# Kernel optimization log

Measured on AMD Instinct MI355X. Metric: run time of the kernel, lower is better.

## Reference

```python
import jax, jax.numpy as jnp
import numpy as np

N_NODES = 100000


def setup_inputs() -> dict:
    key = jax.random.key(0)
    k1, k2, k3 = jax.random.split(key, 3)
    x = jax.random.normal(k1, (N_NODES, 64), dtype=jnp.float32)
    edge_index = jax.random.randint(k2, (2, 1250000), 0, N_NODES, dtype=jnp.int64)
    W = jax.random.normal(k3, (128, 64), dtype=jnp.float32) * (1.0 / np.sqrt(128.0))
    b = jnp.zeros((64,), dtype=jnp.float32)
    return {"x": x, "edge_index": edge_index, "W": W, "b": b}


def reference(x, edge_index, W, b):
    n = x.shape[0]
    row, col = edge_index[0], edge_index[1]
    # scatter-add neighbor features onto destination nodes
    neigh = jax.ops.segment_sum(x[row], col, num_segments=n)          # [n, d]
    count = jax.ops.segment_sum(jnp.ones_like(col, dtype=x.dtype), col, num_segments=n)
    count = jnp.where(count == 0, jnp.asarray(1.0, x.dtype), count)   # avoid div-by-zero
    neigh = neigh / count[:, None]                                    # mean aggregation
    x_aggr = jnp.concatenate([x, neigh], axis=-1)                     # [n, 2d]
    out = x_aggr @ W + b                                              # [n, out_dim]
    return jax.nn.relu(out)  # dropout=0.0 (eval) -> identity
```

## Files before the change

### kernel.cpp

```cpp
#include <hip/hip_runtime.h>

#define D 64
#define NPB 64
#define THREADS 512
#define CAP 64

__device__ __forceinline__ unsigned short f2bf(float f) {
  unsigned u = __float_as_uint(f);
  return (unsigned short)((u + 0x7FFFu + ((u >> 16) & 1u)) >> 16);
}
__device__ __forceinline__ float bf2f(unsigned short h) {
  return __uint_as_float(((unsigned)h) << 16);
}

__global__ __launch_bounds__(256) void cvt_kernel(
    const float* __restrict__ x, ushort* __restrict__ xh, int total4) {
  int t = blockIdx.x * blockDim.x + threadIdx.x;
  if (t >= total4) return;
  float4 v = ((const float4*)x)[t];
  ushort4 h;
  h.x = f2bf(v.x); h.y = f2bf(v.y); h.z = f2bf(v.z); h.w = f2bf(v.w);
  ((ushort4*)xh)[t] = h;
}

__global__ __launch_bounds__(256) void fill_xcd_kernel(
    const int* __restrict__ ei, int* __restrict__ cnt,
    int* __restrict__ bucket, int e, int qpc) {
  const int myx = blockIdx.x & 7;
  const int chunk = blockIdx.x >> 3;
  const int quads = e >> 2;
  const int4* row4 = (const int4*)ei;
  const int4* col4 = (const int4*)(ei + e);
  int qend = chunk * qpc + qpc;
  if (qend > quads) qend = quads;
  for (int q = chunk * qpc + threadIdx.x; q < qend; q += 256) {
    int4 r = row4[q];
    int4 c = col4[q];
    if (((c.x >> 11) & 7) == myx) {
      int p = atomicAdd(&cnt[c.x], 1);
      if (p < CAP) bucket[(size_t)c.x * CAP + p] = r.x;
    }
    if (((c.y >> 11) & 7) == myx) {
      int p = atomicAdd(&cnt[c.y], 1);
      if (p < CAP) bucket[(size_t)c.y * CAP + p] = r.y;
    }
    if (((c.z >> 11) & 7) == myx) {
      int p = atomicAdd(&cnt[c.z], 1);
      if (p < CAP) bucket[(size_t)c.z * CAP + p] = r.z;
    }
    if (((c.w >> 11) & 7) == myx) {
      int p = atomicAdd(&cnt[c.w], 1);
      if (p < CAP) bucket[(size_t)c.w * CAP + p] = r.w;
    }
  }
}

__global__ __launch_bounds__(THREADS, 8) void fused_bf_kernel(
    const float* __restrict__ x, const ushort* __restrict__ xh,
    const int* __restrict__ cnt, const float* __restrict__ W,
    const float* __restrict__ b, float* __restrict__ out, int n) {
  __shared__ __align__(16) float xs[NPB * 128];

  const int lane = threadIdx.x & 63;
  const int wid  = threadIdx.x >> 6;
  const int base = blockIdx.x * NPB;
  const int* bucket = (const int*)out;

  for (int m = 0; m < 8; ++m) {
    int nl = wid * 8 + m;
    int node = base + nl;
    if (node < n) {
      int dg = cnt[node];
      int dc = dg < CAP ? dg : CAP;
      int bk = bucket[(size_t)node * CAP + lane];
      float xown = x[(size_t)node * D + lane];
      float s0 = 0.f, s1 = 0.f, s2 = 0.f, s3 = 0.f;
      float s4 = 0.f, s5 = 0.f, s6 = 0.f, s7 = 0.f;
      int p = 0;
      for (; p + 8 <= dc; p += 8) {
        int a0 = __shfl(bk, p),     a1 = __shfl(bk, p + 1);
        int a2 = __shfl(bk, p + 2), a3 = __shfl(bk, p + 3);
        int a4 = __shfl(bk, p + 4), a5 = __shfl(bk, p + 5);
        int a6 = __shfl(bk, p + 6), a7 = __shfl(bk, p + 7);
        ushort h0 = xh[(size_t)a0 * D + lane];
        ushort h1 = xh[(size_t)a1 * D + lane];
        ushort h2 = xh[(size_t)a2 * D + lane];
        ushort h3 = xh[(size_t)a3 * D + lane];
        ushort h4 = xh[(size_t)a4 * D + lane];
        ushort h5 = xh[(size_t)a5 * D + lane];
        ushort h6 = xh[(size_t)a6 * D + lane];
        ushort h7 = xh[(size_t)a7 * D + lane];
        s0 += bf2f(h0); s1 += bf2f(h1); s2 += bf2f(h2); s3 += bf2f(h3);
        s4 += bf2f(h4); s5 += bf2f(h5); s6 += bf2f(h6); s7 += bf2f(h7);
      }
      for (; p + 4 <= dc; p += 4) {
        int a0 = __shfl(bk, p),     a1 = __shfl(bk, p + 1);
        int a2 = __shfl(bk, p + 2), a3 = __shfl(bk, p + 3);
        ushort h0 = xh[(size_t)a0 * D + lane];
        ushort h1 = xh[(size_t)a1 * D + lane];
        ushort h2 = xh[(size_t)a2 * D + lane];
        ushort h3 = xh[(size_t)a3 * D + lane];
        s0 += bf2f(h0); s1 += bf2f(h1); s2 += bf2f(h2); s3 += bf2f(h3);
      }
      for (; p < dc; ++p)
        s0 += bf2f(xh[(size_t)__shfl(bk, p) * D + lane]);
      float sum = ((s0 + s1) + (s2 + s3)) + ((s4 + s5) + (s6 + s7));
      float inv = (dg > 0) ? (1.0f / (float)dg) : 0.0f;
      xs[nl * 128 + lane]      = xown;
      xs[nl * 128 + 64 + lane] = sum * inv;
    } else {
      xs[nl * 128 + lane]      = 0.0f;
      xs[nl * 128 + 64 + lane] = 0.0f;
    }
  }
  __syncthreads();

  const int col = lane;
  float bias = b[col];
  float acc[8];
#pragma unroll
  for (int m = 0; m < 8; ++m) acc[m] = bias;

  for (int k = 0; k < 128; k += 4) {
    float w0 = W[(k + 0) * 64 + col];
    float w1 = W[(k + 1) * 64 + col];
    float w2 = W[(k + 2) * 64 + col];
    float w3 = W[(k + 3) * 64 + col];
#pragma unroll
    for (int m = 0; m < 8; ++m) {
      int nl = wid + m * 8;
      float4 xv = *(const float4*)&xs[nl * 128 + k];
      acc[m] = fmaf(xv.x, w0, acc[m]);
      acc[m] = fmaf(xv.y, w1, acc[m]);
      acc[m] = fmaf(xv.z, w2, acc[m]);
      acc[m] = fmaf(xv.w, w3, acc[m]);
    }
  }

#pragma unroll
  for (int m = 0; m < 8; ++m) {
    int node = base + wid + m * 8;
    if (node < n)
      out[(size_t)node * D + col] = fmaxf(acc[m], 0.0f);
  }
}

__global__ __launch_bounds__(256) void fill_cap_kernel(
    const int* __restrict__ ei, int* __restrict__ cnt,
    int* __restrict__ bucket, int e) {
  int t = blockIdx.x * blockDim.x + threadIdx.x;
  if (t * 4 >= e) return;
  int4 r4 = ((const int4*)ei)[t];
  int4 c4 = ((const int4*)(ei + e))[t];
  int p0 = atomicAdd(&cnt[c4.x], 1);
  int p1 = atomicAdd(&cnt[c4.y], 1);
  int p2 = atomicAdd(&cnt[c4.z], 1);
  int p3 = atomicAdd(&cnt[c4.w], 1);
  if (p0 < CAP) bucket[(size_t)c4.x * CAP + p0] = r4.x;
  if (p1 < CAP) bucket[(size_t)c4.y * CAP + p1] = r4.y;
  if (p2 < CAP) bucket[(size_t)c4.z * CAP + p2] = r4.z;
  if (p3 < CAP) bucket[(size_t)c4.w * CAP + p3] = r4.w;
}

__global__ __launch_bounds__(THREADS, 8) void fused_cap_kernel(
    const float* __restrict__ x, const int* __restrict__ cnt,
    const float* __restrict__ W, const float* __restrict__ b,
    float* __restrict__ out, int n) {
  __shared__ __align__(16) float xs[NPB * 128];
  const int lane = threadIdx.x & 63;
  const int wid  = threadIdx.x >> 6;
  const int base = blockIdx.x * NPB;
  const int* bucket = (const int*)out;

  for (int m = 0; m < 8; ++m) {
    int nl = wid * 8 + m;
    int node = base + nl;
    if (node < n) {
      int dg = cnt[node];
      int dc = dg < CAP ? dg : CAP;
      int bk = bucket[(size_t)node * CAP + lane];
      float xown = x[(size_t)node * D + lane];
      float s0 = 0.f, s1 = 0.f, s2 = 0.f, s3 = 0.f;
      float s4 = 0.f, s5 = 0.f, s6 = 0.f, s7 = 0.f;
      int p = 0;
      for (; p + 8 <= dc; p += 8) {
        int a0 = __shfl(bk, p),     a1 = __shfl(bk, p + 1);
        int a2 = __shfl(bk, p + 2), a3 = __shfl(bk, p + 3);
        int a4 = __shfl(bk, p + 4), a5 = __shfl(bk, p + 5);
        int a6 = __shfl(bk, p + 6), a7 = __shfl(bk, p + 7);
        s0 += x[(size_t)a0 * D + lane];
        s1 += x[(size_t)a1 * D + lane];
        s2 += x[(size_t)a2 * D + lane];
        s3 += x[(size_t)a3 * D + lane];
        s4 += x[(size_t)a4 * D + lane];
        s5 += x[(size_t)a5 * D + lane];
        s6 += x[(size_t)a6 * D + lane];
        s7 += x[(size_t)a7 * D + lane];
      }
      for (; p + 4 <= dc; p += 4) {
        int a0 = __shfl(bk, p),     a1 = __shfl(bk, p + 1);
        int a2 = __shfl(bk, p + 2), a3 = __shfl(bk, p + 3);
        s0 += x[(size_t)a0 * D + lane];
        s1 += x[(size_t)a1 * D + lane];
        s2 += x[(size_t)a2 * D + lane];
        s3 += x[(size_t)a3 * D + lane];
      }
      for (; p < dc; ++p)
        s0 += x[(size_t)__shfl(bk, p) * D + lane];
      float sum = ((s0 + s1) + (s2 + s3)) + ((s4 + s5) + (s6 + s7));
      float inv = (dg > 0) ? (1.0f / (float)dg) : 0.0f;
      xs[nl * 128 + lane]      = xown;
      xs[nl * 128 + 64 + lane] = sum * inv;
    } else {
      xs[nl * 128 + lane]      = 0.0f;
      xs[nl * 128 + 64 + lane] = 0.0f;
    }
  }
  __syncthreads();

  const int col = lane;
  float bias = b[col];
  float acc[8];
#pragma unroll
  for (int m = 0; m < 8; ++m) acc[m] = bias;
  for (int k = 0; k < 128; k += 4) {
    float w0 = W[(k + 0) * 64 + col];
    float w1 = W[(k + 1) * 64 + col];
    float w2 = W[(k + 2) * 64 + col];
    float w3 = W[(k + 3) * 64 + col];
#pragma unroll
    for (int m = 0; m < 8; ++m) {
      int nl = wid + m * 8;
      float4 xv = *(const float4*)&xs[nl * 128 + k];
      acc[m] = fmaf(xv.x, w0, acc[m]);
      acc[m] = fmaf(xv.y, w1, acc[m]);
      acc[m] = fmaf(xv.z, w2, acc[m]);
      acc[m] = fmaf(xv.w, w3, acc[m]);
    }
  }
#pragma unroll
  for (int m = 0; m < 8; ++m) {
    int node = base + wid + m * 8;
    if (node < n)
      out[(size_t)node * D + col] = fmaxf(acc[m], 0.0f);
  }
}

extern "C" void kernel_launch(void* const* d_in, const int* in_sizes, int n_in,
                              void* d_out, int out_size, void* d_ws, size_t ws_size,
                              hipStream_t stream) {
  const float* x = (const float*)d_in[0];
  const int* ei = (const int*)d_in[1];
  const float* W = (const float*)d_in[2];
  const float* b = (const float*)d_in[3];
  float* out = (float*)d_out;

  int n = in_sizes[0] / D;
  int e = in_sizes[1] / 2;
  int nblocks = (n + NPB - 1) / NPB;

  size_t xh_bytes = (size_t)n * D * sizeof(ushort);
  size_t need = xh_bytes + (size_t)n * sizeof(int) + 256;

  if (ws_size >= need && (e & 3) == 0 && n <= (1 << 17)) {
    ushort* xh = (ushort*)d_ws;
    int* cnt = (int*)((char*)d_ws + ((xh_bytes + 255) & ~(size_t)255));

    int total4 = n * D / 4;
    cvt_kernel<<<(total4 + 255) / 256, 256, 0, stream>>>(x, xh, total4);

    hipMemsetAsync(cnt, 0, (size_t)n * sizeof(int), stream);

    int quads = e >> 2;
    int qpc = (quads + 255) / 256;
    fill_xcd_kernel<<<256 * 8, 256, 0, stream>>>(ei, cnt, (int*)d_out, e, qpc);

    fused_bf_kernel<<<nblocks, THREADS, 0, stream>>>(x, xh, cnt, W, b, out, n);
  } else {
    int* cnt = (int*)d_ws;
    hipMemsetAsync(cnt, 0, (size_t)n * sizeof(int), stream);
    int quads = e / 4;
    fill_cap_kernel<<<(quads + 255) / 256, 256, 0, stream>>>(ei, cnt, (int*)d_out, e);
    fused_cap_kernel<<<nblocks, THREADS, 0, stream>>>(x, cnt, W, b, out, n);
  }
}
```

Measured before the change: 210.1 us.

## Merge prep stages into cooperative kernel and gather two bf16 features per lane

Replaces the separate bf16 conversion kernel, count memset and bucket-fill kernel with one cooperative prep kernel that zeroes counts and converts x, then does a grid-wide sync before filling buckets. This removes two launches and a memset. The gather loop now has each half-wavefront load a 32-bit pair of bf16 values for a different neighbor, so each wave covers two neighbors per load and halves the load instruction count, then combines the halves with a cross-lane xor shuffle. The fallback path drops its 8-way unroll. Risks include the cost of the grid sync, a smaller grid now handling the bucket fill, and per-call occupancy and attribute queries on the host.

```diff
diff --git a/kernel.cpp b/kernel.cpp
--- a/kernel.cpp
+++ b/kernel.cpp
@@ -1,4 +1,7 @@
 #include <hip/hip_runtime.h>
+#include <hip/hip_cooperative_groups.h>
+
+namespace cg = cooperative_groups;
 
 #define D 64
 #define NPB 64
@@ -9,23 +12,25 @@
   unsigned u = __float_as_uint(f);
   return (unsigned short)((u + 0x7FFFu + ((u >> 16) & 1u)) >> 16);
 }
-__device__ __forceinline__ float bf2f(unsigned short h) {
-  return __uint_as_float(((unsigned)h) << 16);
-}
-
-__global__ __launch_bounds__(256) void cvt_kernel(
-    const float* __restrict__ x, ushort* __restrict__ xh, int total4) {
-  int t = blockIdx.x * blockDim.x + threadIdx.x;
-  if (t >= total4) return;
-  float4 v = ((const float4*)x)[t];
-  ushort4 h;
-  h.x = f2bf(v.x); h.y = f2bf(v.y); h.z = f2bf(v.z); h.w = f2bf(v.w);
-  ((ushort4*)xh)[t] = h;
-}
-
-__global__ __launch_bounds__(256) void fill_xcd_kernel(
-    const int* __restrict__ ei, int* __restrict__ cnt,
-    int* __restrict__ bucket, int e, int qpc) {
+
+__global__ __launch_bounds__(256) void prep_kernel(
+    const float* __restrict__ x, const int* __restrict__ ei,
+    ushort* __restrict__ xh, int* __restrict__ cnt,
+    int* __restrict__ bucket, int n, int e, int qpc) {
+  cg::grid_group grid = cg::this_grid();
+  const int tid = blockIdx.x * 256 + threadIdx.x;
+  const int nth = gridDim.x * 256;
+
+  for (int i = tid; i < n; i += nth) cnt[i] = 0;
+  const int total4 = n * D / 4;
+  for (int i = tid; i < total4; i += nth) {
+    float4 v = ((const float4*)x)[i];
+    ushort4 h;
+    h.x = f2bf(v.x); h.y = f2bf(v.y); h.z = f2bf(v.z); h.w = f2bf(v.w);
+    ((ushort4*)xh)[i] = h;
+  }
+  grid.sync();
+
   const int myx = blockIdx.x & 7;
   const int chunk = blockIdx.x >> 3;
   const int quads = e >> 2;
@@ -55,7 +60,7 @@
   }
 }
 
-__global__ __launch_bounds__(THREADS, 8) void fused_bf_kernel(
+__global__ __launch_bounds__(THREADS, 8) void fused2_kernel(
     const float* __restrict__ x, const ushort* __restrict__ xh,
     const int* __restrict__ cnt, const float* __restrict__ W,
     const float* __restrict__ b, float* __restrict__ out, int n) {
@@ -64,7 +69,10 @@
   const int lane = threadIdx.x & 63;
   const int wid  = threadIdx.x >> 6;
   const int base = blockIdx.x * NPB;
+  const int half = lane >> 5;
+  const int fl   = lane & 31;
   const int* bucket = (const int*)out;
+  const ushort* xp = xh + fl * 2;
 
   for (int m = 0; m < 8; ++m) {
     int nl = wid * 8 + m;
@@ -74,40 +82,49 @@
       int dc = dg < CAP ? dg : CAP;
       int bk = bucket[(size_t)node * CAP + lane];
       float xown = x[(size_t)node * D + lane];
-      float s0 = 0.f, s1 = 0.f, s2 = 0.f, s3 = 0.f;
-      float s4 = 0.f, s5 = 0.f, s6 = 0.f, s7 = 0.f;
+      float sl0 = 0.f, sl1 = 0.f, sl2 = 0.f, sl3 = 0.f;
+      float sh0 = 0.f, sh1 = 0.f, sh2 = 0.f, sh3 = 0.f;
       int p = 0;
       for (; p + 8 <= dc; p += 8) {
-        int a0 = __shfl(bk, p),     a1 = __shfl(bk, p + 1);
-        int a2 = __shfl(bk, p + 2), a3 = __shfl(bk, p + 3);
-        int a4 = __shfl(bk, p + 4), a5 = __shfl(bk, p + 5);
-        int a6 = __shfl(bk, p + 6), a7 = __shfl(bk, p + 7);
-        ushort h0 = xh[(size_t)a0 * D + lane];
-        ushort h1 = xh[(size_t)a1 * D + lane];
-        ushort h2 = xh[(size_t)a2 * D + lane];
-        ushort h3 = xh[(size_t)a3 * D + lane];
-        ushort h4 = xh[(size_t)a4 * D + lane];
-        ushort h5 = xh[(size_t)a5 * D + lane];
-        ushort h6 = xh[(size_t)a6 * D + lane];
-        ushort h7 = xh[(size_t)a7 * D + lane];
-        s0 += bf2f(h0); s1 += bf2f(h1); s2 += bf2f(h2); s3 += bf2f(h3);
-        s4 += bf2f(h4); s5 += bf2f(h5); s6 += bf2f(h6); s7 += bf2f(h7);
-      }
-      for (; p + 4 <= dc; p += 4) {
-        int a0 = __shfl(bk, p),     a1 = __shfl(bk, p + 1);
-        int a2 = __shfl(bk, p + 2), a3 = __shfl(bk, p + 3);
-        ushort h0 = xh[(size_t)a0 * D + lane];
-        ushort h1 = xh[(size_t)a1 * D + lane];
-        ushort h2 = xh[(size_t)a2 * D + lane];
-        ushort h3 = xh[(size_t)a3 * D + lane];
-        s0 += bf2f(h0); s1 += bf2f(h1); s2 += bf2f(h2); s3 += bf2f(h3);
-      }
-      for (; p < dc; ++p)
-        s0 += bf2f(xh[(size_t)__shfl(bk, p) * D + lane]);
-      float sum = ((s0 + s1) + (s2 + s3)) + ((s4 + s5) + (s6 + s7));
+        int a0 = __shfl(bk, p + 0 + half);
+        int a1 = __shfl(bk, p + 2 + half);
+        int a2 = __shfl(bk, p + 4 + half);
+        int a3 = __shfl(bk, p + 6 + half);
+        unsigned h0 = *(const unsigned*)(xp + (size_t)a0 * D);
+        unsigned h1 = *(const unsigned*)(xp + (size_t)a1 * D);
+        unsigned h2 = *(const unsigned*)(xp + (size_t)a2 * D);
+        unsigned h3 = *(const unsigned*)(xp + (size_t)a3 * D);
+        sl0 += __uint_as_float(h0 << 16);
+        sh0 += __uint_as_float(h0 & 0xffff0000u);
+        sl1 += __uint_as_float(h1 << 16);
+        sh1 += __uint_as_float(h1 & 0xffff0000u);
+        sl2 += __uint_as_float(h2 << 16);
+        sh2 += __uint_as_float(h2 & 0xffff0000u);
+        sl3 += __uint_as_float(h3 << 16);
+        sh3 += __uint_as_float(h3 & 0xffff0000u);
+      }
+      for (; p + 2 <= dc; p += 2) {
+        int a = __shfl(bk, p + half);
+        unsigned h = *(const unsigned*)(xp + (size_t)a * D);
+        sl0 += __uint_as_float(h << 16);
+        sh0 += __uint_as_float(h & 0xffff0000u);
+      }
+      if (p < dc) {
+        int a = __shfl(bk, p);
+        if (half == 0) {
+          unsigned h = *(const unsigned*)(xp + (size_t)a * D);
+          sl0 += __uint_as_float(h << 16);
+          sh0 += __uint_as_float(h & 0xffff0000u);
+        }
+      }
+      float sl = (sl0 + sl1) + (sl2 + sl3);
+      float sh = (sh0 + sh1) + (sh2 + sh3);
+      sl += __shfl_xor(sl, 32);
+      sh += __shfl_xor(sh, 32);
       float inv = (dg > 0) ? (1.0f / (float)dg) : 0.0f;
-      xs[nl * 128 + lane]      = xown;
-      xs[nl * 128 + 64 + lane] = sum * inv;
+      xs[nl * 128 + lane] = xown;
+      if (half == 0)
+        *(float2*)&xs[nl * 128 + 64 + fl * 2] = make_float2(sl * inv, sh * inv);
     } else {
       xs[nl * 128 + lane]      = 0.0f;
       xs[nl * 128 + 64 + lane] = 0.0f;
@@ -181,22 +198,7 @@
       int bk = bucket[(size_t)node * CAP + lane];
       float xown = x[(size_t)node * D + lane];
       float s0 = 0.f, s1 = 0.f, s2 = 0.f, s3 = 0.f;
-      float s4 = 0.f, s5 = 0.f, s6 = 0.f, s7 = 0.f;
       int p = 0;
-      for (; p + 8 <= dc; p += 8) {
-        int a0 = __shfl(bk, p),     a1 = __shfl(bk, p + 1);
-        int a2 = __shfl(bk, p + 2), a3 = __shfl(bk, p + 3);
-        int a4 = __shfl(bk, p + 4), a5 = __shfl(bk, p + 5);
-        int a6 = __shfl(bk, p + 6), a7 = __shfl(bk, p + 7);
-        s0 += x[(size_t)a0 * D + lane];
-        s1 += x[(size_t)a1 * D + lane];
-        s2 += x[(size_t)a2 * D + lane];
-        s3 += x[(size_t)a3 * D + lane];
-        s4 += x[(size_t)a4 * D + lane];
-        s5 += x[(size_t)a5 * D + lane];
-        s6 += x[(size_t)a6 * D + lane];
-        s7 += x[(size_t)a7 * D + lane];
-      }
       for (; p + 4 <= dc; p += 4) {
         int a0 = __shfl(bk, p),     a1 = __shfl(bk, p + 1);
         int a2 = __shfl(bk, p + 2), a3 = __shfl(bk, p + 3);
@@ -207,7 +209,7 @@
       }
       for (; p < dc; ++p)
         s0 += x[(size_t)__shfl(bk, p) * D + lane];
-      float sum = ((s0 + s1) + (s2 + s3)) + ((s4 + s5) + (s6 + s7));
+      float sum = (s0 + s1) + (s2 + s3);
       float inv = (dg > 0) ? (1.0f / (float)dg) : 0.0f;
       xs[nl * 128 + lane]      = xown;
       xs[nl * 128 + 64 + lane] = sum * inv;
@@ -266,16 +268,24 @@
     ushort* xh = (ushort*)d_ws;
     int* cnt = (int*)((char*)d_ws + ((xh_bytes + 255) & ~(size_t)255));
 
-    int total4 = n * D / 4;
-    cvt_kernel<<<(total4 + 255) / 256, 256, 0, stream>>>(x, xh, total4);
-
-    hipMemsetAsync(cnt, 0, (size_t)n * sizeof(int), stream);
+    int occ = 8, ncu = 256;
+    hipOccupancyMaxActiveBlocksPerMultiprocessor(&occ, prep_kernel, 256, 0);
+    hipDeviceGetAttribute(&ncu, hipDeviceAttributeMultiprocessorCount, 0);
+    long long cap = (long long)occ * ncu;
+    int grid = (int)(cap < 2048 ? cap : 2048);
+    grid &= ~7;
+    if (grid < 8) grid = 8;
 
     int quads = e >> 2;
-    int qpc = (quads + 255) / 256;
-    fill_xcd_kernel<<<256 * 8, 256, 0, stream>>>(ei, cnt, (int*)d_out, e, qpc);
-
-    fused_bf_kernel<<<nblocks, THREADS, 0, stream>>>(x, xh, cnt, W, b, out, n);
+    int nchunks = grid >> 3;
+    int qpc = (quads + nchunks - 1) / nchunks;
+
+    void* args[] = {(void*)&x, (void*)&ei, (void*)&xh, (void*)&cnt,
+                    (void*)&d_out, (void*)&n, (void*)&e, (void*)&qpc};
+    hipLaunchCooperativeKernel((void*)prep_kernel, dim3(grid), dim3(256),
+                               args, 0, stream);
+
+    fused2_kernel<<<nblocks, THREADS, 0, stream>>>(x, xh, cnt, W, b, out, n);
   } else {
     int* cnt = (int*)d_ws;
     hipMemsetAsync(cnt, 0, (size_t)n * sizeof(int), stream);
```

Measured after the change: 365.7 us. +74.0%, slower.
